# Kernel optimization log

Hardware: AMD Instinct MI355X
Metric: run time of the kernel (lower is better)

Reference implementation:

```python
import jax, jax.numpy as jnp
import numpy as np

T, B, K = 512, 512, 8
V, H, NL, NLAB = 5, 30, 4, 3


def setup_inputs() -> dict:
    key = jax.random.key(0)
    ks = jax.random.split(key, 12)
    s = 0.1
    return {
        "x": jax.random.randint(ks[0], (T, B, K), 0, V),
        "weight_of_x": jax.random.uniform(ks[1], (T, B, K), dtype=jnp.float32),
        "embed": jax.random.normal(ks[2], (V, H), dtype=jnp.float32) * s,
        "lstm_Wih": jax.random.normal(ks[3], (NL, 4 * H, H), dtype=jnp.float32) * s,
        "lstm_Whh": jax.random.normal(ks[4], (NL, 4 * H, H), dtype=jnp.float32) * s,
        "lstm_bih": jax.random.normal(ks[5], (NL, 4 * H), dtype=jnp.float32) * s,
        "lstm_bhh": jax.random.normal(ks[6], (NL, 4 * H), dtype=jnp.float32) * s,
        "attn_W1": jax.random.normal(ks[7], (H, 64), dtype=jnp.float32) * s,
        "attn_b1": jnp.zeros((64,), jnp.float32),
        "attn_W2": jax.random.normal(ks[8], (64, 1), dtype=jnp.float32) * s,
        "attn_b2": jnp.zeros((1,), jnp.float32),
        "fc_W": jax.random.normal(ks[9], (H, NLAB), dtype=jnp.float32) * s,
        "fc_b": jnp.zeros((NLAB,), jnp.float32),
    }


def _lstm_layer(xs, Wih, Whh, bih, bhh):
    # xs: (T, B, H_in); PyTorch gate order i, f, g, o
    b = bih + bhh
    Bsz = xs.shape[1]
    h0 = jnp.zeros((Bsz, Whh.shape[1]), xs.dtype)

    def step(carry, xt):
        h, c = carry
        gates = xt @ Wih.T + h @ Whh.T + b  # (B, 4H)
        i, f, g, o = jnp.split(gates, 4, axis=-1)
        i, f, o = jax.nn.sigmoid(i), jax.nn.sigmoid(f), jax.nn.sigmoid(o)
        g = jnp.tanh(g)
        c = f * c + i * g
        h = o * jnp.tanh(c)
        return (h, c), h

    _, hs = jax.lax.scan(step, (h0, h0), xs)
    return hs  # (T, B, H)


def reference(x, weight_of_x, embed, lstm_Wih, lstm_Whh, lstm_bih, lstm_bhh,
              attn_W1, attn_b1, attn_W2, attn_b2, fc_W, fc_b):
    # embedding + weighted mean pooling over K
    e = embed[x] * weight_of_x[..., None]          # (T, B, K, H)
    e = jax.nn.relu(e)
    seq = jnp.mean(e, axis=2)                      # (T, B, H)

    # 4-layer LSTM (loop over fixed num_layers)
    out = seq
    for l in range(lstm_Wih.shape[0]):
        out = _lstm_layer(out, lstm_Wih[l], lstm_Whh[l], lstm_bih[l], lstm_bhh[l])

    # attention pooling over time
    enc = jnp.transpose(out, (1, 0, 2))            # (B, T, H)
    energy = jax.nn.relu(enc @ attn_W1 + attn_b1) @ attn_W2 + attn_b2  # (B, T, 1)
    weights = jax.nn.softmax(energy[..., 0], axis=1)  # (B, T)
    pooled = jnp.sum(enc * weights[..., None], axis=1)  # (B, H)

    # dropout is identity in eval mode
    logit = jax.nn.softmax(pooled @ fc_W + fc_b, axis=1)  # (B, 3)
    return logit
```

## Files before the change

kernel.cpp:

```cpp
#include <hip/hip_runtime.h>

#define TT 512
#define BB 512
#define KK 8
#define HH 30
#define GG 120
#define NLAYER 4

__device__ __forceinline__ float rcp_f(float x) { return __builtin_amdgcn_rcpf(x); }
__device__ __forceinline__ float rdlane_f(float v, int l) {
    return __int_as_float(__builtin_amdgcn_readlane(__float_as_int(v), l));
}
__device__ __forceinline__ float2 pk_fma_s(float2 a, float2 bs, float2 c) {
    float2 d;
    asm("v_pk_fma_f32 %0, %1, %2, %3" : "=v"(d) : "v"(a), "s"(bs), "v"(c));
    return d;
}
__device__ __forceinline__ float2 pk_add(float2 a, float2 b) {
    float2 d;
    asm("v_pk_add_f32 %0, %1, %2" : "=v"(d) : "v"(a), "v"(b));
    return d;
}

__global__ __launch_bounds__(256, 2) void rnn_fused(
    const int*   __restrict__ xin,  const float* __restrict__ wxin,
    const float* __restrict__ embed,
    const float* __restrict__ Wih,  const float* __restrict__ Whh,
    const float* __restrict__ bih,  const float* __restrict__ bhh,
    const float* __restrict__ W1,   const float* __restrict__ b1,
    const float* __restrict__ W2,   const float* __restrict__ b2,
    const float* __restrict__ fcW,  const float* __restrict__ fcb,
    float* __restrict__ out)
{
    __shared__ alignas(16) float hstore[TT * HH];
    __shared__ alignas(16) float seqring[2][16][32];
    __shared__ alignas(16) int   ringx[4][16][KK];
    __shared__ alignas(16) float ringw[4][16][KK];
    __shared__ alignas(16) float hring[3][8][32];
    __shared__ alignas(16) float re_s[5 * HH];
    __shared__ alignas(16) float energy_s[TT];
    __shared__ float red_s[16];
    __shared__ float part_s[8][HH];
    __shared__ float pooled_s[HH];
    __shared__ float logits_s[3];
    __shared__ int   sync_s[8];

    const int tid  = threadIdx.x;
    const int wv   = tid >> 6;
    const int lane = tid & 63;
    const int b    = blockIdx.x;
    volatile int* vs = sync_s;

    if (tid < 8) sync_s[tid] = 0;
    if (tid < 5 * HH) re_s[tid] = fmaxf(embed[tid], 0.0f);

    int4 hx = {0,0,0,0}; float4 hw = {0,0,0,0};
    if (wv == 0 && lane < 32) {
        const int r = lane >> 1, hf = lane & 1;
        #pragma unroll
        for (int cc = 0; cc < 2; ++cc) {
            long off = ((long)(16 * cc + r) * BB + b) * KK + hf * 4;
            *(int4*)(&ringx[cc][r][hf * 4])   = *(const int4*)(xin  + off);
            *(float4*)(&ringw[cc][r][hf * 4]) = *(const float4*)(wxin + off);
        }
        long off2 = ((long)(32 + r) * BB + b) * KK + hf * 4;
        hx = *(const int4*)(xin  + off2);
        hw = *(const float4*)(wxin + off2);
    }

    const int p  = (lane < 60) ? lane : 59;
    const int g0 = p, g1 = p + 60;
    float2 wih0p[15], wih1p[15], whh0p[15], whh1p[15];
    {
        const float* WihL = Wih + wv * GG * HH;
        const float* WhhL = Whh + wv * GG * HH;
        #pragma unroll
        for (int kk = 0; kk < 15; ++kk) {
            wih0p[kk] = *(const float2*)(WihL + g0 * HH + 2 * kk);
            wih1p[kk] = *(const float2*)(WihL + g1 * HH + 2 * kk);
            whh0p[kk] = *(const float2*)(WhhL + g0 * HH + 2 * kk);
            whh1p[kk] = *(const float2*)(WhhL + g1 * HH + 2 * kk);
        }
    }
    const float bias0 = bih[wv * GG + g0] + bhh[wv * GG + g0];
    const float bias1 = bih[wv * GG + g1] + bhh[wv * GG + g1];
    const float mBneg = (lane < HH) ? -2.0f : -1.0f;
    const float aB    = (lane < HH) ?  2.0f :  1.0f;
    const float dB    = (lane < HH) ? -1.0f :  0.0f;

    __syncthreads();

    float c_val = 0.0f;
    float hprev = 0.0f;

    auto do_step = [&](int t) {
        const float* xsrc = (wv == 0) ? &seqring[(t >> 4) & 1][t & 15][0]
                                      : &hring[wv - 1][t & 7][0];
        const float xi = xsrc[lane & 31];
        float2 ah0 = {0.f,0.f}, ah1 = {0.f,0.f};
        #pragma unroll
        for (int k = 0; k < 15; ++k) {
            float2 hp;
            hp.x = rdlane_f(hprev, 2 * k);
            hp.y = rdlane_f(hprev, 2 * k + 1);
            ah0 = pk_fma_s(whh0p[k], hp, ah0);
            ah1 = pk_fma_s(whh1p[k], hp, ah1);
        }
        float2 ax0 = {0.f,0.f}, ax1 = {0.f,0.f};
        #pragma unroll
        for (int k = 0; k < 15; ++k) {
            float2 xp;
            xp.x = rdlane_f(xi, 2 * k);
            xp.y = rdlane_f(xi, 2 * k + 1);
            ax0 = pk_fma_s(wih0p[k], xp, ax0);
            ax1 = pk_fma_s(wih1p[k], xp, ax1);
        }
        const float2 s0 = pk_add(ax0, ah0);
        const float2 s1 = pk_add(ax1, ah1);
        const float gA = s0.x + s0.y + bias0;
        const float gB = s1.x + s1.y + bias1;
        const float actA = rcp_f(1.0f + __expf(-gA));
        const float sB   = rcp_f(1.0f + __expf(gB * mBneg));
        const float actB = fmaf(aB, sB, dB);
        const float fI = __shfl(actA, lane + HH, 64);
        const float oI = __shfl(actB, lane + HH, 64);
        c_val = fmaf(fI, c_val, actA * actB);
        const float tC = fmaf(2.0f, rcp_f(1.0f + __expf(-2.0f * c_val)), -1.0f);
        const float hv = oI * tC;
        hprev = hv;
        if (lane < HH) {
            if (wv < NLAYER - 1) hring[wv][t & 7][lane] = hv;
            else                 hstore[t * HH + lane]  = hv;
        }
    };

    for (int T0 = 0; T0 < TT; T0 += 4) {
        if (wv == 0) {
            if ((T0 & 15) == 0) {
                const int c = T0 >> 4;
                if (lane < 32) {
                    const int r = lane >> 1, hf = lane & 1;
                    if (c <= 29) {
                        const int sl = (c + 2) & 3;
                        *(int4*)(&ringx[sl][r][hf * 4])   = hx;
                        *(float4*)(&ringw[sl][r][hf * 4]) = hw;
                    }
                    if (c <= 28) {
                        long off = ((long)(16 * (c + 3) + r) * BB + b) * KK + hf * 4;
                        hx = *(const int4*)(xin  + off);
                        hw = *(const float4*)(wxin + off);
                    }
                }
                const int sl = c & 3, par = c & 1;
                #pragma unroll
                for (int rr = 0; rr < 8; ++rr) {
                    const int o = lane + rr * 64;
                    if (o < 480) {
                        const int tr = o / HH, j = o - tr * HH;
                        int4   xa = *(const int4*)(&ringx[sl][tr][0]);
                        int4   xb = *(const int4*)(&ringx[sl][tr][4]);
                        float4 wa = *(const float4*)(&ringw[sl][tr][0]);
                        float4 wb = *(const float4*)(&ringw[sl][tr][4]);
                        float acc = re_s[xa.x * HH + j] * wa.x;
                        acc = fmaf(re_s[xa.y * HH + j], wa.y, acc);
                        acc = fmaf(re_s[xa.z * HH + j], wa.z, acc);
                        acc = fmaf(re_s[xa.w * HH + j], wa.w, acc);
                        acc = fmaf(re_s[xb.x * HH + j], wb.x, acc);
                        acc = fmaf(re_s[xb.y * HH + j], wb.y, acc);
                        acc = fmaf(re_s[xb.z * HH + j], wb.z, acc);
                        acc = fmaf(re_s[xb.w * HH + j], wb.w, acc);
                        seqring[par][tr][j] = acc * 0.125f;
                    }
                }
                __threadfence_block();
            }
        } else {
            while (vs[wv - 1] < T0 + 4) __builtin_amdgcn_s_sleep(2);
        }
        if (wv < NLAYER - 1) {
            while (vs[4 + wv + 1] < T0 - 4) __builtin_amdgcn_s_sleep(2);
        }
        __threadfence_block();
        do_step(T0 + 0);
        do_step(T0 + 1);
        do_step(T0 + 2);
        do_step(T0 + 3);
        __threadfence_block();
        if (lane == 0) {
            if (wv < NLAYER - 1) vs[wv]     = T0 + 4;
            if (wv > 0)          vs[4 + wv] = T0 + 4;
        }
    }

    __syncthreads();

    {
        float w1cx[15], w1cy[15];
        #pragma unroll
        for (int k = 0; k < 15; ++k) {
            w1cx[k] = W1[(2 * k) * 64 + lane];
            w1cy[k] = W1[(2 * k + 1) * 64 + lane];
        }
        const float b1v = b1[lane];
        const float w2v = W2[lane];
        const float b2v = b2[0];
        #pragma unroll
        for (int pass = 0; pass < 2; ++pass) {
            const int t = wv * 128 + pass * 64 + lane;
            float2 h2[15];
            #pragma unroll
            for (int k = 0; k < 15; ++k)
                h2[k] = *(const float2*)(hstore + t * HH + 2 * k);
            float e = b2v;
            for (int u = 0; u < 64; ++u) {
                float2 acc = {0.f, 0.f};
                #pragma unroll
                for (int k = 0; k < 15; ++k) {
                    float2 wp;
                    wp.x = rdlane_f(w1cx[k], u);
                    wp.y = rdlane_f(w1cy[k], u);
                    acc = pk_fma_s(h2[k], wp, acc);
                }
                const float su = acc.x + acc.y + rdlane_f(b1v, u);
                e = fmaf(fmaxf(su, 0.0f), rdlane_f(w2v, u), e);
            }
            energy_s[t] = e;
        }
    }
    __syncthreads();

    float mx = -3.0e38f;
    for (int i = tid; i < TT; i += 256) mx = fmaxf(mx, energy_s[i]);
    #pragma unroll
    for (int m = 1; m < 64; m <<= 1) mx = fmaxf(mx, __shfl_xor(mx, m, 64));
    if (lane == 0) red_s[wv] = mx;
    __syncthreads();
    mx = fmaxf(fmaxf(red_s[0], red_s[1]), fmaxf(red_s[2], red_s[3]));
    float ssum = 0.0f;
    for (int i = tid; i < TT; i += 256) {
        float ev = __expf(energy_s[i] - mx);
        energy_s[i] = ev;
        ssum += ev;
    }
    #pragma unroll
    for (int m = 1; m < 64; m <<= 1) ssum += __shfl_xor(ssum, m, 64);
    if (lane == 0) red_s[8 + wv] = ssum;
    __syncthreads();
    const float invS = rcp_f(red_s[8] + red_s[9] + red_s[10] + red_s[11]);

    {
        const int g = tid >> 5, jj = tid & 31;
        if (jj < HH) {
            float part = 0.0f;
            for (int t = g; t < TT; t += 8)
                part = fmaf(energy_s[t] * invS, hstore[t * HH + jj], part);
            part_s[g][jj] = part;
        }
    }
    __syncthreads();
    if (tid < HH) {
        float pv = 0.0f;
        #pragma unroll
        for (int q = 0; q < 8; ++q) pv += part_s[q][tid];
        pooled_s[tid] = pv;
    }
    __syncthreads();

    if (tid < 3) {
        float acc = fcb[tid];
        #pragma unroll
        for (int k = 0; k < HH; ++k) acc = fmaf(pooled_s[k], fcW[k * 3 + tid], acc);
        logits_s[tid] = acc;
    }
    __syncthreads();
    if (tid == 0) {
        float l0 = logits_s[0], l1 = logits_s[1], l2 = logits_s[2];
        float m3 = fmaxf(l0, fmaxf(l1, l2));
        float e0 = __expf(l0 - m3), e1 = __expf(l1 - m3), e2 = __expf(l2 - m3);
        float inv = rcp_f(e0 + e1 + e2);
        out[b * 3 + 0] = e0 * inv; out[b * 3 + 1] = e1 * inv; out[b * 3 + 2] = e2 * inv;
    }
}

extern "C" void kernel_launch(void* const* d_in, const int* in_sizes, int n_in,
                              void* d_out, int out_size, void* d_ws, size_t ws_size,
                              hipStream_t stream)
{
    (void)in_sizes; (void)n_in; (void)d_ws; (void)ws_size; (void)out_size;
    rnn_fused<<<BB, 256, 0, stream>>>(
        (const int*)  d_in[0],  (const float*)d_in[1],  (const float*)d_in[2],
        (const float*)d_in[3],  (const float*)d_in[4],  (const float*)d_in[5],
        (const float*)d_in[6],  (const float*)d_in[7],  (const float*)d_in[8],
        (const float*)d_in[9],  (const float*)d_in[10], (const float*)d_in[11],
        (const float*)d_in[12], (float*)d_out);
}
```

Before: 513.1 us.

## Read LSTM inputs from LDS vectors and use permlane32 swap for gate exchange

```diff
diff --git a/kernel.cpp b/kernel.cpp
--- a/kernel.cpp
+++ b/kernel.cpp
@@ -11,6 +11,11 @@
 __device__ __forceinline__ float rdlane_f(float v, int l) {
     return __int_as_float(__builtin_amdgcn_readlane(__float_as_int(v), l));
 }
+__device__ __forceinline__ float2 pk_fma_v(float2 a, float2 b, float2 c) {
+    float2 d;
+    asm("v_pk_fma_f32 %0, %1, %2, %3" : "=v"(d) : "v"(a), "v"(b), "v"(c));
+    return d;
+}
 __device__ __forceinline__ float2 pk_fma_s(float2 a, float2 bs, float2 c) {
     float2 d;
     asm("v_pk_fma_f32 %0, %1, %2, %3" : "=v"(d) : "v"(a), "s"(bs), "v"(c));
@@ -21,8 +26,14 @@
     asm("v_pk_add_f32 %0, %1, %2" : "=v"(d) : "v"(a), "v"(b));
     return d;
 }
-
-__global__ __launch_bounds__(256, 2) void rnn_fused(
+__device__ __forceinline__ float swap32_hi(float x) {
+    float a = x, b = x;
+    asm("v_permlane32_swap_b32 %0, %1" : "+v"(a), "+v"(b));
+    return b;
+}
+
+__global__ __launch_bounds__(256) __attribute__((amdgpu_waves_per_eu(2, 2)))
+void rnn_fused(
     const int*   __restrict__ xin,  const float* __restrict__ wxin,
     const float* __restrict__ embed,
     const float* __restrict__ Wih,  const float* __restrict__ Whh,
@@ -36,7 +47,7 @@
     __shared__ alignas(16) float seqring[2][16][32];
     __shared__ alignas(16) int   ringx[4][16][KK];
     __shared__ alignas(16) float ringw[4][16][KK];
-    __shared__ alignas(16) float hring[3][8][32];
+    __shared__ alignas(16) float hring[NLAYER][8][32];
     __shared__ alignas(16) float re_s[5 * HH];
     __shared__ alignas(16) float energy_s[TT];
     __shared__ float red_s[16];
@@ -53,6 +64,10 @@
 
     if (tid < 8) sync_s[tid] = 0;
     if (tid < 5 * HH) re_s[tid] = fmaxf(embed[tid], 0.0f);
+    {
+        float4 z; z.x = 0.f; z.y = 0.f; z.z = 0.f; z.w = 0.f;
+        ((float4*)hring)[tid] = z;
+    }
 
     int4 hx = {0,0,0,0}; float4 hw = {0,0,0,0};
     if (wv == 0 && lane < 32) {
@@ -68,69 +83,63 @@
         hw = *(const float4*)(wxin + off2);
     }
 
-    const int p  = (lane < 60) ? lane : 59;
-    const int g0 = p, g1 = p + 60;
-    float2 wih0p[15], wih1p[15], whh0p[15], whh1p[15];
+    const int half = lane >> 5;
+    const int q31  = lane & 31;
+    const int qq   = (q31 < HH) ? q31 : (HH - 1);
+    const int rA   = qq + half * HH;
+    const int rB   = rA + 60;
+    float2 wihA[15], wihB[15], whhA[15], whhB[15];
     {
         const float* WihL = Wih + wv * GG * HH;
         const float* WhhL = Whh + wv * GG * HH;
         #pragma unroll
         for (int kk = 0; kk < 15; ++kk) {
-            wih0p[kk] = *(const float2*)(WihL + g0 * HH + 2 * kk);
-            wih1p[kk] = *(const float2*)(WihL + g1 * HH + 2 * kk);
-            whh0p[kk] = *(const float2*)(WhhL + g0 * HH + 2 * kk);
-            whh1p[kk] = *(const float2*)(WhhL + g1 * HH + 2 * kk);
-        }
-    }
-    const float bias0 = bih[wv * GG + g0] + bhh[wv * GG + g0];
-    const float bias1 = bih[wv * GG + g1] + bhh[wv * GG + g1];
-    const float mBneg = (lane < HH) ? -2.0f : -1.0f;
-    const float aB    = (lane < HH) ?  2.0f :  1.0f;
-    const float dB    = (lane < HH) ? -1.0f :  0.0f;
+            wihA[kk] = *(const float2*)(WihL + rA * HH + 2 * kk);
+            wihB[kk] = *(const float2*)(WihL + rB * HH + 2 * kk);
+            whhA[kk] = *(const float2*)(WhhL + rA * HH + 2 * kk);
+            whhB[kk] = *(const float2*)(WhhL + rB * HH + 2 * kk);
+        }
+    }
+    const float biasA = bih[wv * GG + rA] + bhh[wv * GG + rA];
+    const float biasB = bih[wv * GG + rB] + bhh[wv * GG + rB];
+    const float mBneg = (lane < 32) ? -2.0f : -1.0f;
+    const float aB    = (lane < 32) ?  2.0f :  1.0f;
+    const float dB    = (lane < 32) ? -1.0f :  0.0f;
 
     __syncthreads();
 
     float c_val = 0.0f;
-    float hprev = 0.0f;
 
     auto do_step = [&](int t) {
         const float* xsrc = (wv == 0) ? &seqring[(t >> 4) & 1][t & 15][0]
                                       : &hring[wv - 1][t & 7][0];
-        const float xi = xsrc[lane & 31];
+        const float* hsrc = &hring[wv][(t + 7) & 7][0];
         float2 ah0 = {0.f,0.f}, ah1 = {0.f,0.f};
+        float2 ax0 = {0.f,0.f}, ax1 = {0.f,0.f};
         #pragma unroll
         for (int k = 0; k < 15; ++k) {
-            float2 hp;
-            hp.x = rdlane_f(hprev, 2 * k);
-            hp.y = rdlane_f(hprev, 2 * k + 1);
-            ah0 = pk_fma_s(whh0p[k], hp, ah0);
-            ah1 = pk_fma_s(whh1p[k], hp, ah1);
-        }
-        float2 ax0 = {0.f,0.f}, ax1 = {0.f,0.f};
-        #pragma unroll
-        for (int k = 0; k < 15; ++k) {
-            float2 xp;
-            xp.x = rdlane_f(xi, 2 * k);
-            xp.y = rdlane_f(xi, 2 * k + 1);
-            ax0 = pk_fma_s(wih0p[k], xp, ax0);
-            ax1 = pk_fma_s(wih1p[k], xp, ax1);
+            const float2 xp = *(const float2*)(xsrc + 2 * k);
+            const float2 hp = *(const float2*)(hsrc + 2 * k);
+            ax0 = pk_fma_v(wihA[k], xp, ax0);
+            ax1 = pk_fma_v(wihB[k], xp, ax1);
+            ah0 = pk_fma_v(whhA[k], hp, ah0);
+            ah1 = pk_fma_v(whhB[k], hp, ah1);
         }
         const float2 s0 = pk_add(ax0, ah0);
         const float2 s1 = pk_add(ax1, ah1);
-        const float gA = s0.x + s0.y + bias0;
-        const float gB = s1.x + s1.y + bias1;
+        const float gA = s0.x + s0.y + biasA;
+        const float gB = s1.x + s1.y + biasB;
         const float actA = rcp_f(1.0f + __expf(-gA));
         const float sB   = rcp_f(1.0f + __expf(gB * mBneg));
         const float actB = fmaf(aB, sB, dB);
-        const float fI = __shfl(actA, lane + HH, 64);
-        const float oI = __shfl(actB, lane + HH, 64);
+        const float fI = swap32_hi(actA);
+        const float oI = swap32_hi(actB);
         c_val = fmaf(fI, c_val, actA * actB);
         const float tC = fmaf(2.0f, rcp_f(1.0f + __expf(-2.0f * c_val)), -1.0f);
         const float hv = oI * tC;
-        hprev = hv;
         if (lane < HH) {
-            if (wv < NLAYER - 1) hring[wv][t & 7][lane] = hv;
-            else                 hstore[t * HH + lane]  = hv;
+            hring[wv][t & 7][lane] = hv;
+            if (wv == NLAYER - 1) hstore[t * HH + lane] = hv;
         }
     };
 
```

Result: faster. 496.9 us (-3.2%).
